# Performance work log

Measured on AMD Instinct MI355X. Metric: run time of the kernel, lower is better.

## Reference

```python
import jax, jax.numpy as jnp
import numpy as np
import math

N_HEADS = 16

def setup_inputs() -> dict:
    key = jax.random.key(0)
    ks = jax.random.split(key, 5)
    B, S, D = 4, 2048, 1024
    scale = 0.02
    return {
        "x": jax.random.normal(ks[0], (B, S, D), dtype=jnp.float32),
        "w_in": jax.random.normal(ks[1], (D, 3 * D), dtype=jnp.float32) * scale,
        "b_in": jax.random.normal(ks[2], (3 * D,), dtype=jnp.float32) * scale,
        "w_out": jax.random.normal(ks[3], (D, D), dtype=jnp.float32) * scale,
        "b_out": jax.random.normal(ks[4], (D,), dtype=jnp.float32) * scale,
    }

def reference(x, w_in, b_in, w_out, b_out):
    B, S, D = x.shape
    H = N_HEADS
    dh = D // H
    qkv = x @ w_in + b_in                      # [B,S,3D]
    q, k, v = jnp.split(qkv, 3, axis=-1)
    # [B,S,D] -> [B,H,S,dh]
    q = q.reshape(B, S, H, dh).transpose(0, 2, 1, 3)
    k = k.reshape(B, S, H, dh).transpose(0, 2, 1, 3)
    v = v.reshape(B, S, H, dh).transpose(0, 2, 1, 3)
    scores = jnp.einsum("bhqd,bhkd->bhqk", q, k) / math.sqrt(dh)
    causal = jnp.tril(jnp.ones((S, S), dtype=bool))  # allow k <= q
    scores = jnp.where(causal, scores, -jnp.inf)
    wei = jax.nn.softmax(scores, axis=-1)
    out = jnp.einsum("bhqk,bhkd->bhqd", wei, v)      # [B,H,S,dh]
    out = out.transpose(0, 2, 1, 3).reshape(B, S, D)
    return out @ w_out + b_out
```

## Files before the change

### kernel.cpp

```cpp
#include <hip/hip_runtime.h>

typedef unsigned short u16;
typedef unsigned int   u32;
typedef float  f32x4  __attribute__((ext_vector_type(4)));
typedef __bf16 bf16x8 __attribute__((ext_vector_type(8)));
typedef __bf16 bf16x4 __attribute__((ext_vector_type(4)));
typedef short  s16x4  __attribute__((ext_vector_type(4)));
typedef unsigned short u16x8 __attribute__((ext_vector_type(8)));
typedef unsigned int   u32x4 __attribute__((ext_vector_type(4)));

__device__ __forceinline__ u16 f2bf(float f) {
  u32 u = __builtin_bit_cast(u32, f);
  u = (u + 0x7fffu + ((u >> 16) & 1u)) >> 16;
  return (u16)u;
}

__device__ __forceinline__ void gload_lds16(const void* g, void* l) {
  __builtin_amdgcn_global_load_lds(
      (const __attribute__((address_space(1))) void*)g,
      (__attribute__((address_space(3))) void*)l, 16, 0, 0);
}

#define VMCNT6() asm volatile("s_waitcnt vmcnt(6)" ::: "memory")
#define VMCNT0() asm volatile("s_waitcnt vmcnt(0)" ::: "memory")

__global__ __launch_bounds__(256) void conv_f32_bf16(
    const float* __restrict__ in, u16* __restrict__ out, int n8) {
  int i = blockIdx.x * 256 + threadIdx.x;
  if (i >= n8) return;
  const float4* p = (const float4*)in;
  float4 a = p[2 * i], b = p[2 * i + 1];
  u16x8 r;
  r[0] = f2bf(a.x); r[1] = f2bf(a.y); r[2] = f2bf(a.z); r[3] = f2bf(a.w);
  r[4] = f2bf(b.x); r[5] = f2bf(b.y); r[6] = f2bf(b.z); r[7] = f2bf(b.w);
  ((u16x8*)out)[i] = r;
}

__global__ __launch_bounds__(256) void conv_transpose(
    const float* __restrict__ in, u16* __restrict__ out, int K, int N) {
  __shared__ float tile[64][65];
  int nb = N >> 6;
  int tk = blockIdx.x / nb, tn = blockIdx.x % nb;
  int t = threadIdx.x;
  int kl = t >> 4, n4 = (t & 15) * 4;
#pragma unroll
  for (int i = 0; i < 4; ++i) {
    int k = kl + 16 * i;
    float4 v = *(const float4*)(in + (size_t)(tk * 64 + k) * N + tn * 64 + n4);
    tile[k][n4] = v.x; tile[k][n4 + 1] = v.y; tile[k][n4 + 2] = v.z; tile[k][n4 + 3] = v.w;
  }
  __syncthreads();
  int nl = t >> 4, k4 = (t & 15) * 4;
#pragma unroll
  for (int i = 0; i < 4; ++i) {
    int n = nl + 16 * i;
    ushort4 o;
    o.x = f2bf(tile[k4 + 0][n]); o.y = f2bf(tile[k4 + 1][n]);
    o.z = f2bf(tile[k4 + 2][n]); o.w = f2bf(tile[k4 + 3][n]);
    *(ushort4*)(out + (size_t)(tn * 64 + n) * K + tk * 64 + k4) = o;
  }
}

template <int OUT_BF16, int SCALE_Q>
__global__ __launch_bounds__(512, 2) void gemm3b(
    const u16* __restrict__ A, const u16* __restrict__ Bt,
    const float* __restrict__ bias, void* __restrict__ C,
    int M, int N, int K) {
  __shared__ __align__(16) char smem[3][49152];
  int tid = threadIdx.x, w = tid >> 6, lane = tid & 63;
  int g = lane >> 4, l15 = lane & 15, l7 = lane & 7, l8 = lane >> 3;
  int wm = w >> 2, wn = w & 3;
  int cpx = (int)gridDim.x >> 3;
  int bid = (blockIdx.x & 7) * cpx + (blockIdx.x >> 3);
  int nblk = N >> 7;
  int bm = bid / nblk, bn = bid % nblk;
  int m0 = bm << 8, n0 = bn << 7;

  auto stageAB = [&](int buf, int kt) {
#pragma unroll
    for (int i = 0; i < 4; ++i) {
      int row = w * 32 + i * 8 + l8;
      const u16* src = A + (size_t)(m0 + row) * K + kt * 64 + 8 * (l7 ^ (row & 7));
      gload_lds16(src, &smem[buf][(w * 32 + i * 8) * 128]);
    }
#pragma unroll
    for (int i = 0; i < 2; ++i) {
      int row = w * 16 + i * 8 + l8;
      const u16* src = Bt + (size_t)(n0 + row) * K + kt * 64 + 8 * (l7 ^ (row & 7));
      gload_lds16(src, &smem[buf][32768 + (w * 16 + i * 8) * 128]);
    }
  };
  auto ldA = [&](int buf, int mh, int mi, int kk) -> bf16x8 {
    int row = mh * 128 + wm * 64 + mi * 16 + l15;
    return *(const bf16x8*)&smem[buf][row * 128 + (((kk * 4 + g) * 16) ^ ((row & 7) << 4))];
  };
  auto ldB = [&](int buf, int ni, int kk) -> bf16x8 {
    int row = wn * 32 + ni * 16 + l15;
    return *(const bf16x8*)&smem[buf][32768 + row * 128 + (((kk * 4 + g) * 16) ^ ((row & 7) << 4))];
  };

  f32x4 acc[2][4][2];
#pragma unroll
  for (int mh = 0; mh < 2; ++mh)
#pragma unroll
    for (int mi = 0; mi < 4; ++mi)
#pragma unroll
      for (int ni = 0; ni < 2; ++ni) acc[mh][mi][ni] = f32x4{0.f, 0.f, 0.f, 0.f};

  const int NT = K >> 6;
  stageAB(0, 0);
  stageAB(1, 1);

  int rb = 0;
  for (int t = 0; t < NT; ++t) {
    if (t < NT - 1) VMCNT6(); else VMCNT0();
    __builtin_amdgcn_s_barrier();
    if (t + 2 < NT) {
      int sb = rb + 2; if (sb >= 3) sb -= 3;
      stageAB(sb, t + 2);
    }

    bf16x8 af[4][2], b0f[2], b1f[2];
#pragma unroll
    for (int mi = 0; mi < 4; ++mi)
#pragma unroll
      for (int kk = 0; kk < 2; ++kk) af[mi][kk] = ldA(rb, 0, mi, kk);
#pragma unroll
    for (int kk = 0; kk < 2; ++kk) b0f[kk] = ldB(rb, 0, kk);
    __builtin_amdgcn_s_setprio(1);
#pragma unroll
    for (int mi = 0; mi < 4; ++mi)
#pragma unroll
      for (int kk = 0; kk < 2; ++kk)
        acc[0][mi][0] = __builtin_amdgcn_mfma_f32_16x16x32_bf16(af[mi][kk], b0f[kk], acc[0][mi][0], 0, 0, 0);
    __builtin_amdgcn_s_setprio(0);
#pragma unroll
    for (int kk = 0; kk < 2; ++kk) b1f[kk] = ldB(rb, 1, kk);
    __builtin_amdgcn_s_setprio(1);
#pragma unroll
    for (int mi = 0; mi < 4; ++mi)
#pragma unroll
      for (int kk = 0; kk < 2; ++kk)
        acc[0][mi][1] = __builtin_amdgcn_mfma_f32_16x16x32_bf16(af[mi][kk], b1f[kk], acc[0][mi][1], 0, 0, 0);
    __builtin_amdgcn_s_setprio(0);
#pragma unroll
    for (int mi = 0; mi < 4; ++mi)
#pragma unroll
      for (int kk = 0; kk < 2; ++kk) af[mi][kk] = ldA(rb, 1, mi, kk);
    __builtin_amdgcn_s_setprio(1);
#pragma unroll
    for (int mi = 0; mi < 4; ++mi)
#pragma unroll
      for (int kk = 0; kk < 2; ++kk)
        acc[1][mi][1] = __builtin_amdgcn_mfma_f32_16x16x32_bf16(af[mi][kk], b1f[kk], acc[1][mi][1], 0, 0, 0);
    __builtin_amdgcn_s_setprio(0);
    __builtin_amdgcn_s_setprio(1);
#pragma unroll
    for (int mi = 0; mi < 4; ++mi)
#pragma unroll
      for (int kk = 0; kk < 2; ++kk)
        acc[1][mi][0] = __builtin_amdgcn_mfma_f32_16x16x32_bf16(af[mi][kk], b0f[kk], acc[1][mi][0], 0, 0, 0);
    __builtin_amdgcn_s_setprio(0);

    ++rb; if (rb >= 3) rb -= 3;
  }

#pragma unroll
  for (int ni = 0; ni < 2; ++ni) {
    int col = n0 + wn * 32 + ni * 16 + l15;
    float bv = bias[col];
    float sc = (SCALE_Q && col < 1024) ? 0.18033688011112042f : 1.0f;
#pragma unroll
    for (int mh = 0; mh < 2; ++mh)
#pragma unroll
      for (int mi = 0; mi < 4; ++mi) {
        int rowb = m0 + mh * 128 + wm * 64 + mi * 16 + g * 4;
#pragma unroll
        for (int r = 0; r < 4; ++r) {
          float v = (acc[mh][mi][ni][r] + bv) * sc;
          if (OUT_BF16)
            ((u16*)C)[(size_t)(rowb + r) * N + col] = f2bf(v);
          else
            ((float*)C)[(size_t)(rowb + r) * N + col] = v;
        }
      }
  }
}


#if __has_builtin(__builtin_amdgcn_mfma_f32_16x16x16bf16_1k)
#define HAVE_MFMA16 1
__device__ __forceinline__ f32x4 mfma16(s16x4 a, s16x4 b, f32x4 c) {
  return __builtin_amdgcn_mfma_f32_16x16x16bf16_1k(a, b, c, 0, 0, 0);
}
#endif

struct V2reg { u16x8 a, b; };

__device__ __forceinline__ void stage_k(const u16* qb, char* kbuf, int kvt,
                                        int h, int w, int lane) {
  int l7 = lane & 7;
#pragma unroll
  for (int i = 0; i < 2; ++i) {
    int rbase = w * 16 + i * 8;
    int row = rbase + (lane >> 3);
    const u16* src = qb + (size_t)(kvt * 64 + row) * 3072 + 1024 + h * 64 + 8 * (l7 ^ (row & 7));
    gload_lds16(src, kbuf + rbase * 128);
  }
}

__device__ __forceinline__ V2reg load_v(const u16* qb, int kvt, int h, int kv0, int d0) {
  const u16* vs = qb + (size_t)(kvt * 64 + kv0) * 3072 + 2048 + h * 64 + d0;
  V2reg r;
  r.a = *(const u16x8*)vs;
  r.b = *(const u16x8*)(vs + 3072);
  return r;
}

__device__ __forceinline__ void write_v(char* vbuf, V2reg v, int kv0, int d0) {
#pragma unroll
  for (int j = 0; j < 8; ++j) {
    int d = d0 + j;
    u32 val = (u32)v.a[j] | ((u32)v.b[j] << 16);
    int sw = ((d & 7) ^ (d >> 3)) << 4;
    *(u32*)(vbuf + d * 128 + ((2 * kv0) ^ sw)) = val;
  }
}

__global__ __launch_bounds__(256, 4) void attn_fwd(
    const u16* __restrict__ qkv, u16* __restrict__ aout) {
  const int S = 2048, D3 = 3072;
  int bh = blockIdx.x & 63;
  int qt = 31 - (blockIdx.x >> 6);
  int b = bh >> 4, h = bh & 15;
  const u16* qb = qkv + (size_t)b * S * D3;

  int tid = threadIdx.x;
  int w = tid >> 6, lane = tid & 63;
  int g = lane >> 4, l15 = lane & 15, l7 = lane & 7;

  __shared__ __align__(16) char Kb[2][8192];
  __shared__ __align__(16) char Vb[2][8192];

  int qrow = qt * 64 + w * 16 + l15;
  const u16* qp = qb + (size_t)qrow * D3 + h * 64 + g * 8;
  bf16x8 qf0 = *(const bf16x8*)qp;
  bf16x8 qf1 = *(const bf16x8*)(qp + 32);

  f32x4 oaT[4];
#pragma unroll
  for (int i = 0; i < 4; ++i) oaT[i] = f32x4{0.f, 0.f, 0.f, 0.f};
  f32x4 l_acc = {0.f, 0.f, 0.f, 0.f};
  float m_s = -3e38f;

  int vkv0 = w * 16 + ((lane >> 3) << 1);
  int vd0 = l7 * 8;

  stage_k(qb, Kb[0], 0, h, w, lane);
  {
    V2reg v = load_v(qb, 0, h, vkv0, vd0);
    write_v(Vb[0], v, vkv0, vd0);
  }
  __syncthreads();

  V2reg vreg;
  for (int kvt = 0; kvt <= qt; ++kvt) {
    int cur = kvt & 1;
    if (kvt < qt) {
      stage_k(qb, Kb[cur ^ 1], kvt + 1, h, w, lane);
      vreg = load_v(qb, kvt + 1, h, vkv0, vd0);
    }

    f32x4 sT[4];
    __builtin_amdgcn_s_setprio(1);
#pragma unroll
    for (int nb = 0; nb < 4; ++nb) {
      int kv = nb * 16 + l15;
      const char* kb = Kb[cur] + kv * 128;
      int sw = (kv & 7) << 4;
      bf16x8 kf0 = *(const bf16x8*)(kb + ((g * 16) ^ sw));
      bf16x8 kf1 = *(const bf16x8*)(kb + ((64 + g * 16) ^ sw));
      f32x4 z = {0.f, 0.f, 0.f, 0.f};
      z = __builtin_amdgcn_mfma_f32_16x16x32_bf16(kf0, qf0, z, 0, 0, 0);
      z = __builtin_amdgcn_mfma_f32_16x16x32_bf16(kf1, qf1, z, 0, 0, 0);
      sT[nb] = z;
    }
    __builtin_amdgcn_s_setprio(0);

    if (kvt == qt) {
      int qloc = w * 16 + l15;
#pragma unroll
      for (int nb = 0; nb < 4; ++nb)
#pragma unroll
        for (int r = 0; r < 4; ++r)
          if (nb * 16 + g * 4 + r > qloc) sT[nb][r] = -1e30f;
    }

    float pm = -3e38f;
#pragma unroll
    for (int nb = 0; nb < 4; ++nb)
#pragma unroll
      for (int r = 0; r < 4; ++r) pm = fmaxf(pm, sT[nb][r]);
    pm = fmaxf(pm, __shfl_xor(pm, 16));
    pm = fmaxf(pm, __shfl_xor(pm, 32));
    if (!__all(pm - m_s <= 8.0f)) {
      float newm = fmaxf(m_s, pm);
      float corr = __builtin_amdgcn_exp2f(m_s - newm);
      m_s = newm;
      l_acc[0] *= corr;
#pragma unroll
      for (int db = 0; db < 4; ++db)
#pragma unroll
        for (int r = 0; r < 4; ++r) oaT[db][r] *= corr;
    }
#pragma unroll
    for (int nb = 0; nb < 4; ++nb)
#pragma unroll
      for (int r = 0; r < 4; ++r)
        sT[nb][r] = __builtin_amdgcn_exp2f(sT[nb][r] - m_s);

#ifdef HAVE_MFMA16
    s16x4 pf[4];
#pragma unroll
    for (int nb = 0; nb < 4; ++nb) {
      bf16x4 t;
#pragma unroll
      for (int r = 0; r < 4; ++r) t[r] = (__bf16)sT[nb][r];
      pf[nb] = __builtin_bit_cast(s16x4, t);
    }
    s16x4 ones;
#pragma unroll
    for (int r = 0; r < 4; ++r) ones[r] = (short)0x3F80;
    __builtin_amdgcn_s_setprio(1);
#pragma unroll
    for (int nb = 0; nb < 4; ++nb) l_acc = mfma16(ones, pf[nb], l_acc);
#pragma unroll
    for (int db = 0; db < 4; ++db) {
      int d = db * 16 + l15;
      const char* vb = Vb[cur] + d * 128;
      int swd = ((d & 7) ^ (d >> 3)) << 4;
#pragma unroll
      for (int nb = 0; nb < 4; ++nb) {
        bf16x4 vf = *(const bf16x4*)(vb + ((nb * 32 + g * 8) ^ swd));
        oaT[db] = mfma16(__builtin_bit_cast(s16x4, vf), pf[nb], oaT[db]);
      }
    }
    __builtin_amdgcn_s_setprio(0);
#else
    u32 wlo[4], whi[4];
#pragma unroll
    for (int nb = 0; nb < 4; ++nb) {
      wlo[nb] = (u32)f2bf(sT[nb][0]) | ((u32)f2bf(sT[nb][1]) << 16);
      whi[nb] = (u32)f2bf(sT[nb][2]) | ((u32)f2bf(sT[nb][3]) << 16);
    }
    int srcA = (2 * (g & 1)) * 16 + l15;
    int srcB = srcA + 16;
    bool hi = (g >> 1) != 0;
    bf16x8 ones8;
#pragma unroll
    for (int j = 0; j < 8; ++j) ones8[j] = __builtin_bit_cast(__bf16, (u16)0x3F80);
    __builtin_amdgcn_s_setprio(1);
#pragma unroll
    for (int kb2 = 0; kb2 < 2; ++kb2) {
      int nbE = kb2 * 2, nbO = kb2 * 2 + 1;
      u32 a0 = __shfl(wlo[nbE], srcA), a1 = __shfl(whi[nbE], srcA);
      u32 a2 = __shfl(wlo[nbE], srcB), a3 = __shfl(whi[nbE], srcB);
      u32 b0 = __shfl(wlo[nbO], srcA), b1 = __shfl(whi[nbO], srcA);
      u32 b2 = __shfl(wlo[nbO], srcB), b3 = __shfl(whi[nbO], srcB);
      u32x4 ow = {hi ? b0 : a0, hi ? b1 : a1, hi ? b2 : a2, hi ? b3 : a3};
      bf16x8 pfrag = __builtin_bit_cast(bf16x8, ow);
      l_acc = __builtin_amdgcn_mfma_f32_16x16x32_bf16(ones8, pfrag, l_acc, 0, 0, 0);
#pragma unroll
      for (int db = 0; db < 4; ++db) {
        int d = db * 16 + l15;
        int swd = ((d & 7) ^ (d >> 3)) << 4;
        bf16x8 vf = *(const bf16x8*)(Vb[cur] + d * 128 + ((kb2 * 64 + g * 16) ^ swd));
        oaT[db] = __builtin_amdgcn_mfma_f32_16x16x32_bf16(vf, pfrag, oaT[db], 0, 0, 0);
      }
    }
    __builtin_amdgcn_s_setprio(0);
#endif

    if (kvt < qt) {
      write_v(Vb[cur ^ 1], vreg, vkv0, vd0);
      __syncthreads();
    }
  }

  float inv = 1.0f / l_acc[0];
  size_t obase = (size_t)(b * S + qt * 64 + w * 16 + l15) * 1024 + h * 64;
#pragma unroll
  for (int db = 0; db < 4; ++db) {
    ushort4 st;
    st.x = f2bf(oaT[db][0] * inv);
    st.y = f2bf(oaT[db][1] * inv);
    st.z = f2bf(oaT[db][2] * inv);
    st.w = f2bf(oaT[db][3] * inv);
    *(ushort4*)(aout + obase + db * 16 + g * 4) = st;
  }
}

extern "C" void kernel_launch(void* const* d_in, const int* in_sizes, int n_in,
                              void* d_out, int out_size, void* d_ws, size_t ws_size,
                              hipStream_t stream) {
  (void)in_sizes; (void)n_in; (void)out_size;
  const float* x     = (const float*)d_in[0];
  const float* w_in  = (const float*)d_in[1];
  const float* b_in  = (const float*)d_in[2];
  const float* w_out = (const float*)d_in[3];
  const float* b_out = (const float*)d_in[4];
  float* out = (float*)d_out;
  char* ws = (char*)d_ws;
  if (ws_size < 92274688u) return;

  u16* xb     = (u16*)(ws);
  u16* w_inT  = (u16*)(ws + (16u << 20));
  u16* w_outT = (u16*)(ws + (22u << 20));
  u16* qkv    = (u16*)(ws + (24u << 20));
  u16* aout   = (u16*)(ws + (72u << 20));

  conv_f32_bf16<<<4096, 256, 0, stream>>>(x, xb, 1048576);
  conv_transpose<<<768, 256, 0, stream>>>(w_in, w_inT, 1024, 3072);
  conv_transpose<<<256, 256, 0, stream>>>(w_out, w_outT, 1024, 1024);
  gemm3b<1, 1><<<768, 512, 0, stream>>>(xb, w_inT, b_in, qkv, 8192, 3072, 1024);
  attn_fwd<<<2048, 256, 0, stream>>>(qkv, aout);
  gemm3b<0, 0><<<256, 512, 0, stream>>>(aout, w_outT, b_out, out, 8192, 1024, 1024);
}
```

Before: 257.1 us.

## Process two adjacent 64-row query tiles per attention block to reuse K/V loads

Each attention workgroup now handles two consecutive 64-row query tiles (128 rows) and shares each staged K/V tile between them, so the grid is halved. It is meant to cut global K/V traffic and LDS staging per query row by reusing each loaded tile for twice the work. In exchange it doubles the accumulator and score registers per thread, which may reduce occupancy under the launch bounds, and it adds branches for the tile that ends one iteration early.

```diff
diff --git a/kernel.cpp b/kernel.cpp
--- a/kernel.cpp
+++ b/kernel.cpp
@@ -231,7 +231,7 @@
     const u16* __restrict__ qkv, u16* __restrict__ aout) {
   const int S = 2048, D3 = 3072;
   int bh = blockIdx.x & 63;
-  int qt = 31 - (blockIdx.x >> 6);
+  int qt = 15 - (blockIdx.x >> 6);
   int b = bh >> 4, h = bh & 15;
   const u16* qb = qkv + (size_t)b * S * D3;
 
@@ -242,20 +242,24 @@
   __shared__ __align__(16) char Kb[2][8192];
   __shared__ __align__(16) char Vb[2][8192];
 
-  int qrow = qt * 64 + w * 16 + l15;
-  const u16* qp = qb + (size_t)qrow * D3 + h * 64 + g * 8;
-  bf16x8 qf0 = *(const bf16x8*)qp;
-  bf16x8 qf1 = *(const bf16x8*)(qp + 32);
-
-  f32x4 oaT[4];
-#pragma unroll
-  for (int i = 0; i < 4; ++i) oaT[i] = f32x4{0.f, 0.f, 0.f, 0.f};
-  f32x4 l_acc = {0.f, 0.f, 0.f, 0.f};
-  float m_s = -3e38f;
+  int qrowA = qt * 128 + w * 16 + l15;
+  const u16* qpA = qb + (size_t)qrowA * D3 + h * 64 + g * 8;
+  bf16x8 qfA0 = *(const bf16x8*)qpA;
+  bf16x8 qfA1 = *(const bf16x8*)(qpA + 32);
+  const u16* qpB = qpA + (size_t)64 * D3;
+  bf16x8 qfB0 = *(const bf16x8*)qpB;
+  bf16x8 qfB1 = *(const bf16x8*)(qpB + 32);
+
+  f32x4 oaTA[4], oaTB[4];
+#pragma unroll
+  for (int i = 0; i < 4; ++i) { oaTA[i] = f32x4{0.f, 0.f, 0.f, 0.f}; oaTB[i] = f32x4{0.f, 0.f, 0.f, 0.f}; }
+  f32x4 lA = {0.f, 0.f, 0.f, 0.f}, lB = {0.f, 0.f, 0.f, 0.f};
+  float mA = -3e38f, mB = -3e38f;
 
   int vkv0 = w * 16 + ((lane >> 3) << 1);
   int vd0 = l7 * 8;
 
+  const int NTk = 2 * qt + 2;
   stage_k(qb, Kb[0], 0, h, w, lane);
   {
     V2reg v = load_v(qb, 0, h, vkv0, vd0);
@@ -264,14 +268,17 @@
   __syncthreads();
 
   V2reg vreg;
-  for (int kvt = 0; kvt <= qt; ++kvt) {
+  for (int kvt = 0; kvt < NTk; ++kvt) {
     int cur = kvt & 1;
-    if (kvt < qt) {
+    if (kvt + 1 < NTk) {
       stage_k(qb, Kb[cur ^ 1], kvt + 1, h, w, lane);
       vreg = load_v(qb, kvt + 1, h, vkv0, vd0);
     }
-
-    f32x4 sT[4];
+    bool doA = (kvt < NTk - 1);
+    bool diagA = (kvt == NTk - 2);
+    bool diagB = (kvt == NTk - 1);
+
+    f32x4 sA[4], sB[4];
     __builtin_amdgcn_s_setprio(1);
 #pragma unroll
     for (int nb = 0; nb < 4; ++nb) {
@@ -280,60 +287,113 @@
       int sw = (kv & 7) << 4;
       bf16x8 kf0 = *(const bf16x8*)(kb + ((g * 16) ^ sw));
       bf16x8 kf1 = *(const bf16x8*)(kb + ((64 + g * 16) ^ sw));
+      if (doA) {
+        f32x4 z = {0.f, 0.f, 0.f, 0.f};
+        z = __builtin_amdgcn_mfma_f32_16x16x32_bf16(kf0, qfA0, z, 0, 0, 0);
+        z = __builtin_amdgcn_mfma_f32_16x16x32_bf16(kf1, qfA1, z, 0, 0, 0);
+        sA[nb] = z;
+      }
       f32x4 z = {0.f, 0.f, 0.f, 0.f};
-      z = __builtin_amdgcn_mfma_f32_16x16x32_bf16(kf0, qf0, z, 0, 0, 0);
-      z = __builtin_amdgcn_mfma_f32_16x16x32_bf16(kf1, qf1, z, 0, 0, 0);
-      sT[nb] = z;
+      z = __builtin_amdgcn_mfma_f32_16x16x32_bf16(kf0, qfB0, z, 0, 0, 0);
+      z = __builtin_amdgcn_mfma_f32_16x16x32_bf16(kf1, qfB1, z, 0, 0, 0);
+      sB[nb] = z;
     }
     __builtin_amdgcn_s_setprio(0);
 
-    if (kvt == qt) {
+    if (diagA) {
       int qloc = w * 16 + l15;
 #pragma unroll
       for (int nb = 0; nb < 4; ++nb)
 #pragma unroll
         for (int r = 0; r < 4; ++r)
-          if (nb * 16 + g * 4 + r > qloc) sT[nb][r] = -1e30f;
-    }
-
-    float pm = -3e38f;
-#pragma unroll
-    for (int nb = 0; nb < 4; ++nb)
-#pragma unroll
-      for (int r = 0; r < 4; ++r) pm = fmaxf(pm, sT[nb][r]);
-    pm = fmaxf(pm, __shfl_xor(pm, 16));
-    pm = fmaxf(pm, __shfl_xor(pm, 32));
-    if (!__all(pm - m_s <= 8.0f)) {
-      float newm = fmaxf(m_s, pm);
-      float corr = __builtin_amdgcn_exp2f(m_s - newm);
-      m_s = newm;
-      l_acc[0] *= corr;
-#pragma unroll
-      for (int db = 0; db < 4; ++db)
-#pragma unroll
-        for (int r = 0; r < 4; ++r) oaT[db][r] *= corr;
-    }
-#pragma unroll
-    for (int nb = 0; nb < 4; ++nb)
-#pragma unroll
-      for (int r = 0; r < 4; ++r)
-        sT[nb][r] = __builtin_amdgcn_exp2f(sT[nb][r] - m_s);
+          if (nb * 16 + g * 4 + r > qloc) sA[nb][r] = -1e30f;
+    }
+    if (diagB) {
+      int qloc = w * 16 + l15;
+#pragma unroll
+      for (int nb = 0; nb < 4; ++nb)
+#pragma unroll
+        for (int r = 0; r < 4; ++r)
+          if (nb * 16 + g * 4 + r > qloc) sB[nb][r] = -1e30f;
+    }
+
+    if (doA) {
+      float pm = -3e38f;
+#pragma unroll
+      for (int nb = 0; nb < 4; ++nb)
+#pragma unroll
+        for (int r = 0; r < 4; ++r) pm = fmaxf(pm, sA[nb][r]);
+      pm = fmaxf(pm, __shfl_xor(pm, 16));
+      pm = fmaxf(pm, __shfl_xor(pm, 32));
+      if (!__all(pm - mA <= 8.0f)) {
+        float newm = fmaxf(mA, pm);
+        float corr = __builtin_amdgcn_exp2f(mA - newm);
+        mA = newm;
+        lA[0] *= corr;
+#pragma unroll
+        for (int db = 0; db < 4; ++db)
+#pragma unroll
+          for (int r = 0; r < 4; ++r) oaTA[db][r] *= corr;
+      }
+#pragma unroll
+      for (int nb = 0; nb < 4; ++nb)
+#pragma unroll
+        for (int r = 0; r < 4; ++r)
+          sA[nb][r] = __builtin_amdgcn_exp2f(sA[nb][r] - mA);
+    }
+    {
+      float pm = -3e38f;
+#pragma unroll
+      for (int nb = 0; nb < 4; ++nb)
+#pragma unroll
+        for (int r = 0; r < 4; ++r) pm = fmaxf(pm, sB[nb][r]);
+      pm = fmaxf(pm, __shfl_xor(pm, 16));
+      pm = fmaxf(pm, __shfl_xor(pm, 32));
+      if (!__all(pm - mB <= 8.0f)) {
+        float newm = fmaxf(mB, pm);
+        float corr = __builtin_amdgcn_exp2f(mB - newm);
+        mB = newm;
+        lB[0] *= corr;
+#pragma unroll
+        for (int db = 0; db < 4; ++db)
+#pragma unroll
+          for (int r = 0; r < 4; ++r) oaTB[db][r] *= corr;
+      }
+#pragma unroll
+      for (int nb = 0; nb < 4; ++nb)
+#pragma unroll
+        for (int r = 0; r < 4; ++r)
+          sB[nb][r] = __builtin_amdgcn_exp2f(sB[nb][r] - mB);
+    }
 
 #ifdef HAVE_MFMA16
-    s16x4 pf[4];
+    s16x4 pfA[4], pfB[4];
+    if (doA) {
+#pragma unroll
+      for (int nb = 0; nb < 4; ++nb) {
+        bf16x4 t;
+#pragma unroll
+        for (int r = 0; r < 4; ++r) t[r] = (__bf16)sA[nb][r];
+        pfA[nb] = __builtin_bit_cast(s16x4, t);
+      }
+    }
 #pragma unroll
     for (int nb = 0; nb < 4; ++nb) {
       bf16x4 t;
 #pragma unroll
-      for (int r = 0; r < 4; ++r) t[r] = (__bf16)sT[nb][r];
-      pf[nb] = __builtin_bit_cast(s16x4, t);
+      for (int r = 0; r < 4; ++r) t[r] = (__bf16)sB[nb][r];
+      pfB[nb] = __builtin_bit_cast(s16x4, t);
     }
     s16x4 ones;
 #pragma unroll
     for (int r = 0; r < 4; ++r) ones[r] = (short)0x3F80;
     __builtin_amdgcn_s_setprio(1);
-#pragma unroll
-    for (int nb = 0; nb < 4; ++nb) l_acc = mfma16(ones, pf[nb], l_acc);
+    if (doA) {
+#pragma unroll
+      for (int nb = 0; nb < 4; ++nb) lA = mfma16(ones, pfA[nb], lA);
+    }
+#pragma unroll
+    for (int nb = 0; nb < 4; ++nb) lB = mfma16(ones, pfB[nb], lB);
 #pragma unroll
     for (int db = 0; db < 4; ++db) {
       int d = db * 16 + l15;
@@ -342,61 +402,74 @@
 #pragma unroll
       for (int nb = 0; nb < 4; ++nb) {
         bf16x4 vf = *(const bf16x4*)(vb + ((nb * 32 + g * 8) ^ swd));
-        oaT[db] = mfma16(__builtin_bit_cast(s16x4, vf), pf[nb], oaT[db]);
+        s16x4 vs = __builtin_bit_cast(s16x4, vf);
+        if (doA) oaTA[db] = mfma16(vs, pfA[nb], oaTA[db]);
+        oaTB[db] = mfma16(vs, pfB[nb], oaTB[db]);
       }
     }
     __builtin_amdgcn_s_setprio(0);
 #else
-    u32 wlo[4], whi[4];
-#pragma unroll
-    for (int nb = 0; nb < 4; ++nb) {
-      wlo[nb] = (u32)f2bf(sT[nb][0]) | ((u32)f2bf(sT[nb][1]) << 16);
-      whi[nb] = (u32)f2bf(sT[nb][2]) | ((u32)f2bf(sT[nb][3]) << 16);
-    }
-    int srcA = (2 * (g & 1)) * 16 + l15;
-    int srcB = srcA + 16;
+    bf16x8 ones8;
+#pragma unroll
+    for (int j = 0; j < 8; ++j) ones8[j] = __builtin_bit_cast(__bf16, (u16)0x3F80);
+    int srcA_ = (2 * (g & 1)) * 16 + l15;
+    int srcB_ = srcA_ + 16;
     bool hi = (g >> 1) != 0;
-    bf16x8 ones8;
-#pragma unroll
-    for (int j = 0; j < 8; ++j) ones8[j] = __builtin_bit_cast(__bf16, (u16)0x3F80);
-    __builtin_amdgcn_s_setprio(1);
-#pragma unroll
-    for (int kb2 = 0; kb2 < 2; ++kb2) {
-      int nbE = kb2 * 2, nbO = kb2 * 2 + 1;
-      u32 a0 = __shfl(wlo[nbE], srcA), a1 = __shfl(whi[nbE], srcA);
-      u32 a2 = __shfl(wlo[nbE], srcB), a3 = __shfl(whi[nbE], srcB);
-      u32 b0 = __shfl(wlo[nbO], srcA), b1 = __shfl(whi[nbO], srcA);
-      u32 b2 = __shfl(wlo[nbO], srcB), b3 = __shfl(whi[nbO], srcB);
-      u32x4 ow = {hi ? b0 : a0, hi ? b1 : a1, hi ? b2 : a2, hi ? b3 : a3};
-      bf16x8 pfrag = __builtin_bit_cast(bf16x8, ow);
-      l_acc = __builtin_amdgcn_mfma_f32_16x16x32_bf16(ones8, pfrag, l_acc, 0, 0, 0);
-#pragma unroll
-      for (int db = 0; db < 4; ++db) {
-        int d = db * 16 + l15;
-        int swd = ((d & 7) ^ (d >> 3)) << 4;
-        bf16x8 vf = *(const bf16x8*)(Vb[cur] + d * 128 + ((kb2 * 64 + g * 16) ^ swd));
-        oaT[db] = __builtin_amdgcn_mfma_f32_16x16x32_bf16(vf, pfrag, oaT[db], 0, 0, 0);
-      }
-    }
-    __builtin_amdgcn_s_setprio(0);
+    for (int grp = 0; grp < 2; ++grp) {
+      if (grp == 0 && !doA) continue;
+      f32x4* sT = (grp == 0) ? sA : sB;
+      f32x4* oaT = (grp == 0) ? oaTA : oaTB;
+      f32x4& l_acc = (grp == 0) ? lA : lB;
+      u32 wlo[4], whi[4];
+#pragma unroll
+      for (int nb = 0; nb < 4; ++nb) {
+        wlo[nb] = (u32)f2bf(sT[nb][0]) | ((u32)f2bf(sT[nb][1]) << 16);
+        whi[nb] = (u32)f2bf(sT[nb][2]) | ((u32)f2bf(sT[nb][3]) << 16);
+      }
+#pragma unroll
+      for (int kb2 = 0; kb2 < 2; ++kb2) {
+        int nbE = kb2 * 2, nbO = kb2 * 2 + 1;
+        u32 a0 = __shfl(wlo[nbE], srcA_), a1 = __shfl(whi[nbE], srcA_);
+        u32 a2 = __shfl(wlo[nbE], srcB_), a3 = __shfl(whi[nbE], srcB_);
+        u32 b0 = __shfl(wlo[nbO], srcA_), b1 = __shfl(whi[nbO], srcA_);
+        u32 b2 = __shfl(wlo[nbO], srcB_), b3 = __shfl(whi[nbO], srcB_);
+        u32x4 ow = {hi ? b0 : a0, hi ? b1 : a1, hi ? b2 : a2, hi ? b3 : a3};
+        bf16x8 pfrag = __builtin_bit_cast(bf16x8, ow);
+        l_acc = __builtin_amdgcn_mfma_f32_16x16x32_bf16(ones8, pfrag, l_acc, 0, 0, 0);
+#pragma unroll
+        for (int db = 0; db < 4; ++db) {
+          int d = db * 16 + l15;
+          int swd = ((d & 7) ^ (d >> 3)) << 4;
+          bf16x8 vf = *(const bf16x8*)(Vb[cur] + d * 128 + ((kb2 * 64 + g * 16) ^ swd));
+          oaT[db] = __builtin_amdgcn_mfma_f32_16x16x32_bf16(vf, pfrag, oaT[db], 0, 0, 0);
+        }
+      }
+    }
 #endif
 
-    if (kvt < qt) {
+    if (kvt + 1 < NTk) {
       write_v(Vb[cur ^ 1], vreg, vkv0, vd0);
       __syncthreads();
     }
   }
 
-  float inv = 1.0f / l_acc[0];
-  size_t obase = (size_t)(b * S + qt * 64 + w * 16 + l15) * 1024 + h * 64;
+  float invA = 1.0f / lA[0];
+  float invB = 1.0f / lB[0];
+  size_t obaseA = (size_t)(b * S + qt * 128 + w * 16 + l15) * 1024 + h * 64;
+  size_t obaseB = obaseA + (size_t)64 * 1024;
 #pragma unroll
   for (int db = 0; db < 4; ++db) {
     ushort4 st;
-    st.x = f2bf(oaT[db][0] * inv);
-    st.y = f2bf(oaT[db][1] * inv);
-    st.z = f2bf(oaT[db][2] * inv);
-    st.w = f2bf(oaT[db][3] * inv);
-    *(ushort4*)(aout + obase + db * 16 + g * 4) = st;
+    st.x = f2bf(oaTA[db][0] * invA);
+    st.y = f2bf(oaTA[db][1] * invA);
+    st.z = f2bf(oaTA[db][2] * invA);
+    st.w = f2bf(oaTA[db][3] * invA);
+    *(ushort4*)(aout + obaseA + db * 16 + g * 4) = st;
+    st.x = f2bf(oaTB[db][0] * invB);
+    st.y = f2bf(oaTB[db][1] * invB);
+    st.z = f2bf(oaTB[db][2] * invB);
+    st.w = f2bf(oaTB[db][3] * invB);
+    *(ushort4*)(aout + obaseB + db * 16 + g * 4) = st;
   }
 }
 
@@ -423,6 +496,6 @@
   conv_transpose<<<768, 256, 0, stream>>>(w_in, w_inT, 1024, 3072);
   conv_transpose<<<256, 256, 0, stream>>>(w_out, w_outT, 1024, 1024);
   gemm3b<1, 1><<<768, 512, 0, stream>>>(xb, w_inT, b_in, qkv, 8192, 3072, 1024);
-  attn_fwd<<<2048, 256, 0, stream>>>(qkv, aout);
+  attn_fwd<<<1024, 256, 0, stream>>>(qkv, aout);
   gemm3b<0, 0><<<256, 512, 0, stream>>>(aout, w_outT, b_out, out, 8192, 1024, 1024);
 }
```

After: 340.1 us. +32.3%, slower.
